# Kernel tuning notes

Measured on AMD Instinct MI355X. Metric: run time of the kernel, lower is better.

The kernel has to match this reference:

```python
import jax, jax.numpy as jnp
import numpy as np

D_MODEL = 1024
N_HEADS = 16
N_KV_HEADS = 4
HEAD_DIM = 64


def setup_inputs() -> dict:
    key = jax.random.key(0)
    ks = jax.random.split(key, 5)
    B, T, P = 2, 512, 8
    scale = 1.0 / np.sqrt(D_MODEL)
    return {
        "hidden_states": jax.random.normal(ks[0], (B, T, P, D_MODEL), dtype=jnp.float32),
        # weights stored [in, out] so y = x @ W (same math as nn.Linear with W^T)
        "Wq": jax.random.normal(ks[1], (D_MODEL, N_HEADS * HEAD_DIM), dtype=jnp.float32) * scale,
        "Wk": jax.random.normal(ks[2], (D_MODEL, N_KV_HEADS * HEAD_DIM), dtype=jnp.float32) * scale,
        "Wv": jax.random.normal(ks[3], (D_MODEL, N_KV_HEADS * HEAD_DIM), dtype=jnp.float32) * scale,
        "Wo": jax.random.normal(ks[4], (N_HEADS * HEAD_DIM, D_MODEL), dtype=jnp.float32) * scale,
    }


def _rope_tables(T, d):
    half = d // 2
    inv_freq = 1.0 / (10000.0 ** (jnp.arange(half, dtype=jnp.float32) / half))
    pos = jnp.arange(T, dtype=jnp.float32)
    angles = pos[:, None] * inv_freq[None, :]  # (T, half)
    return jnp.cos(angles), jnp.sin(angles)


def _apply_rope(x, cos, sin):
    # x: (B, P, T, H, d); cos/sin: (T, d/2)
    half = x.shape[-1] // 2
    x1, x2 = x[..., :half], x[..., half:]
    c = cos[None, None, :, None, :]
    s = sin[None, None, :, None, :]
    return jnp.concatenate([x1 * c - x2 * s, x1 * s + x2 * c], axis=-1)


def reference(hidden_states, Wq, Wk, Wv, Wo):
    B, T, P, _ = hidden_states.shape
    x = jnp.transpose(hidden_states, (0, 2, 1, 3))  # (B, P, T, C)
    q = (x @ Wq).reshape(B, P, T, N_HEADS, HEAD_DIM)
    k = (x @ Wk).reshape(B, P, T, N_KV_HEADS, HEAD_DIM)
    v = (x @ Wv).reshape(B, P, T, N_KV_HEADS, HEAD_DIM)

    rep = N_HEADS // N_KV_HEADS
    k = jnp.repeat(k, rep, axis=3)  # (B,P,T,H,d) interleaved like torch repeat/view
    v = jnp.repeat(v, rep, axis=3)

    cos, sin = _rope_tables(T, HEAD_DIM)
    q = _apply_rope(q, cos, sin)
    k = _apply_rope(k, cos, sin)

    # (B,P,H,T,d)
    q = jnp.transpose(q, (0, 1, 3, 2, 4))
    k = jnp.transpose(k, (0, 1, 3, 2, 4))
    v = jnp.transpose(v, (0, 1, 3, 2, 4))

    attn = jnp.einsum("bphqd,bphkd->bphqk", q, k) / jnp.sqrt(
        jnp.asarray(HEAD_DIM, q.dtype))
    attn = jax.nn.softmax(attn, axis=-1)
    out = jnp.einsum("bphqk,bphkd->bphqd", attn, v)
    out = jnp.transpose(out, (0, 1, 3, 2, 4)).reshape(B, P, T, N_HEADS * HEAD_DIM)
    out = jnp.transpose(out, (0, 2, 1, 3))  # (B, T, P, H*d)
    return out @ Wo
```

## Files before the change

kernel.cpp:

```cpp
#include <hip/hip_runtime.h>
#include <stdint.h>


typedef __attribute__((ext_vector_type(8))) short bf16x8;
typedef __attribute__((ext_vector_type(4))) float f32x4;
typedef __attribute__((ext_vector_type(16))) float f32x16;
typedef __attribute__((ext_vector_type(4))) unsigned short us4;
typedef __attribute__((ext_vector_type(8))) unsigned short us8;

static __device__ __forceinline__ unsigned short f2bf(float f) {
  unsigned u = __float_as_uint(f);
  u += 0x7fffu + ((u >> 16) & 1u);
  return (unsigned short)(u >> 16);
}

static __device__ __forceinline__ void ld_lds16(const void* g, void* l) {
  __builtin_amdgcn_global_load_lds(
      (const __attribute__((address_space(1))) void*)g,
      (__attribute__((address_space(3))) void*)l, 16, 0, 0);
}

static __device__ __forceinline__ f32x4 mfma16(bf16x8 a, bf16x8 b, f32x4 c) {
  return __builtin_amdgcn_mfma_f32_16x16x32_bf16(a, b, c, 0, 0, 0);
}
static __device__ __forceinline__ f32x16 mfma32(bf16x8 a, bf16x8 b, f32x16 c) {
  return __builtin_amdgcn_mfma_f32_32x32x16_bf16(a, b, c, 0, 0, 0);
}

__global__ __launch_bounds__(256) void conv_all(
    const float* __restrict__ hs, const float* __restrict__ Wq,
    const float* __restrict__ Wk, const float* __restrict__ Wv,
    const float* __restrict__ Wo, unsigned short* __restrict__ xb,
    unsigned short* __restrict__ wqkv, unsigned short* __restrict__ wot) {
  __shared__ float tile[64][65];
  int bid = blockIdx.x, tid = threadIdx.x;
  if (bid < 8192) {
    int gid = bid * 256 + tid;
    size_t e = (size_t)gid * 4;
    int r = (int)(e >> 10);
    int d = (int)(e & 1023);
    int b = r >> 12, p = (r >> 9) & 7, t = r & 511;
    const float4* src = (const float4*)(hs + ((((size_t)b * 512 + t) * 8 + p) << 10) + d);
    float4 v = *src;
    us4 o;
    o.x = f2bf(v.x); o.y = f2bf(v.y); o.z = f2bf(v.z); o.w = f2bf(v.w);
    *(us4*)(xb + e) = o;
    return;
  }
  int tb = bid - 8192;
  const float* W; unsigned short* Wt; int N, tc0, tn0;
  if (tb < 256)      { W = Wq; Wt = wqkv;                       N = 1024; tc0 = (tb >> 4) * 64;          tn0 = (tb & 15) * 64; }
  else if (tb < 320) { W = Wk; Wt = wqkv + (size_t)1024 * 1024; N = 256;  tc0 = ((tb - 256) >> 2) * 64;  tn0 = ((tb - 256) & 3) * 64; }
  else if (tb < 384) { W = Wv; Wt = wqkv + (size_t)1280 * 1024; N = 256;  tc0 = ((tb - 320) >> 2) * 64;  tn0 = ((tb - 320) & 3) * 64; }
  else               { W = Wo; Wt = wot;                        N = 1024; tc0 = ((tb - 384) >> 4) * 64;  tn0 = ((tb - 384) & 15) * 64; }
  int tr = tid >> 4, tc = tid & 15;
#pragma unroll
  for (int i = 0; i < 4; ++i) {
    int c = tr + i * 16;
    float4 v = *(const float4*)(W + (size_t)(tc0 + c) * N + tn0 + tc * 4);
    tile[c][tc * 4 + 0] = v.x; tile[c][tc * 4 + 1] = v.y;
    tile[c][tc * 4 + 2] = v.z; tile[c][tc * 4 + 3] = v.w;
  }
  __syncthreads();
#pragma unroll
  for (int i = 0; i < 4; ++i) {
    int n = tr + i * 16;
    us4 o;
    o.x = f2bf(tile[tc * 4 + 0][n]); o.y = f2bf(tile[tc * 4 + 1][n]);
    o.z = f2bf(tile[tc * 4 + 2][n]); o.w = f2bf(tile[tc * 4 + 3][n]);
    *(us4*)(Wt + (size_t)(tn0 + n) * 1024 + tc0 + tc * 4) = o;
  }
}

template <int NT, int MODE>
__global__ __launch_bounds__(512, 2) void gemm256(
    const unsigned short* __restrict__ A, const unsigned short* __restrict__ Bt,
    unsigned short* __restrict__ qb, unsigned short* __restrict__ kb,
    unsigned short* __restrict__ vtb, float* __restrict__ out) {
  constexpr int K = 1024;
  constexpr int KT = K / 64;
  __shared__ __align__(16) unsigned short Sm[2][2][256 * 64];
  unsigned short* Cs = &Sm[0][0][0];

  int tid = threadIdx.x;
  int lane = tid & 63, wid = tid >> 6;
  int quad = lane >> 4, lo = lane & 15;
  int tn = blockIdx.x % NT, tm = blockIdx.x / NT;
  int wr = wid >> 2, wc = wid & 3;
  int srow = lane >> 3, schunk = lane & 7;
  int cg = schunk ^ srow;

  const unsigned short* pa = A + ((size_t)(tm * 256) + wid * 8 + srow) * K + cg * 8;
  const unsigned short* pb = Bt + ((size_t)(tn * 256) + wid * 8 + srow) * K + cg * 8;

  f32x4 z = {0.f, 0.f, 0.f, 0.f};
  f32x4 acc[8][4];
#pragma unroll
  for (int i = 0; i < 8; ++i)
#pragma unroll
    for (int j = 0; j < 4; ++j) acc[i][j] = z;

  auto stage = [&](int t, int p) {
#pragma unroll
    for (int i = 0; i < 4; ++i) {
      ld_lds16(pa + (size_t)i * 64 * K + t * 64,
               (char*)&Sm[p][0][0] + (wid * 8 + i * 64) * 128);
      ld_lds16(pb + (size_t)i * 64 * K + t * 64,
               (char*)&Sm[p][1][0] + (wid * 8 + i * 64) * 128);
    }
  };

  stage(0, 0);
  stage(1, 1);
  asm volatile("s_waitcnt vmcnt(8)" ::: "memory");
  asm volatile("s_barrier" ::: "memory");

  bf16x8 af[4][2], bb0[2][2], bb1[2][2];

  for (int t = 0; t < KT; ++t) {
    int p = t & 1;
    const unsigned short* As = &Sm[p][0][0];
    const unsigned short* Bs = &Sm[p][1][0];

#pragma unroll
    for (int mi = 0; mi < 4; ++mi)
#pragma unroll
      for (int kx = 0; kx < 2; ++kx) {
        int row = wr * 128 + mi * 16 + lo;
        int cgx = (quad + kx * 4) ^ (row & 7);
        af[mi][kx] = *(const bf16x8*)(As + (size_t)row * 64 + cgx * 8);
      }
#pragma unroll
    for (int ni = 0; ni < 2; ++ni)
#pragma unroll
      for (int kx = 0; kx < 2; ++kx) {
        int row = wc * 64 + ni * 16 + lo;
        int cgx = (quad + kx * 4) ^ (row & 7);
        bb0[ni][kx] = *(const bf16x8*)(Bs + (size_t)row * 64 + cgx * 8);
      }
    asm volatile("s_barrier" ::: "memory");
    __builtin_amdgcn_s_setprio(1);
#pragma unroll
    for (int kx = 0; kx < 2; ++kx)
#pragma unroll
      for (int mi = 0; mi < 4; ++mi)
#pragma unroll
        for (int ni = 0; ni < 2; ++ni)
          acc[mi][ni] = mfma16(af[mi][kx], bb0[ni][kx], acc[mi][ni]);
    __builtin_amdgcn_s_setprio(0);
    asm volatile("s_barrier" ::: "memory");

#pragma unroll
    for (int ni = 0; ni < 2; ++ni)
#pragma unroll
      for (int kx = 0; kx < 2; ++kx) {
        int row = wc * 64 + (ni + 2) * 16 + lo;
        int cgx = (quad + kx * 4) ^ (row & 7);
        bb1[ni][kx] = *(const bf16x8*)(Bs + (size_t)row * 64 + cgx * 8);
      }
    asm volatile("s_barrier" ::: "memory");
    __builtin_amdgcn_s_setprio(1);
#pragma unroll
    for (int kx = 0; kx < 2; ++kx)
#pragma unroll
      for (int mi = 0; mi < 4; ++mi)
#pragma unroll
        for (int ni = 0; ni < 2; ++ni)
          acc[mi][ni + 2] = mfma16(af[mi][kx], bb1[ni][kx], acc[mi][ni + 2]);
    __builtin_amdgcn_s_setprio(0);
    asm volatile("s_barrier" ::: "memory");

#pragma unroll
    for (int mi = 0; mi < 4; ++mi)
#pragma unroll
      for (int kx = 0; kx < 2; ++kx) {
        int row = wr * 128 + 64 + mi * 16 + lo;
        int cgx = (quad + kx * 4) ^ (row & 7);
        af[mi][kx] = *(const bf16x8*)(As + (size_t)row * 64 + cgx * 8);
      }
    asm volatile("s_barrier" ::: "memory");
    __builtin_amdgcn_s_setprio(1);
#pragma unroll
    for (int kx = 0; kx < 2; ++kx)
#pragma unroll
      for (int mi = 0; mi < 4; ++mi)
#pragma unroll
        for (int ni = 0; ni < 2; ++ni)
          acc[mi + 4][ni + 2] = mfma16(af[mi][kx], bb1[ni][kx], acc[mi + 4][ni + 2]);
    __builtin_amdgcn_s_setprio(0);
    asm volatile("s_barrier" ::: "memory");

    bool pf = (t + 2 < KT);
    if (pf) stage(t + 2, p);
    __builtin_amdgcn_s_setprio(1);
#pragma unroll
    for (int kx = 0; kx < 2; ++kx)
#pragma unroll
      for (int mi = 0; mi < 4; ++mi)
#pragma unroll
        for (int ni = 0; ni < 2; ++ni)
          acc[mi + 4][ni] = mfma16(af[mi][kx], bb0[ni][kx], acc[mi + 4][ni]);
    __builtin_amdgcn_s_setprio(0);
    if (pf) asm volatile("s_waitcnt vmcnt(8)" ::: "memory");
    else    asm volatile("s_waitcnt vmcnt(0)" ::: "memory");
    asm volatile("s_barrier" ::: "memory");
  }

  if (MODE == 0 && tn < 5) {
    float qscale = (tn < 4) ? 0.125f : 1.0f;
#pragma unroll
    for (int mi = 0; mi < 8; ++mi)
#pragma unroll
      for (int r = 0; r < 4; ++r) {
        int row = wr * 128 + mi * 16 + quad * 4 + r;
        int tpos = (tm * 256 + row) & 511;
#pragma unroll
        for (int ni = 0; ni < 2; ++ni) {
          float invf = exp2f((float)(ni * 16 + lo) * -0.41524101186092029f);
          float ang = (float)tpos * invf;
          float s, c;
          __sincosf(ang, &s, &c);
          float x1 = acc[mi][ni][r], x2 = acc[mi][ni + 2][r];
          acc[mi][ni][r]     = (x1 * c - x2 * s) * qscale;
          acc[mi][ni + 2][r] = (x1 * s + x2 * c) * qscale;
        }
      }
#pragma unroll
    for (int mi = 0; mi < 8; ++mi)
#pragma unroll
      for (int ni = 0; ni < 4; ++ni)
#pragma unroll
        for (int r = 0; r < 4; ++r) {
          int row = wr * 128 + mi * 16 + quad * 4 + r;
          int col = wc * 64 + ni * 16 + lo;
          int cs = col ^ (((row >> 2) & 3) << 3);
          Cs[row * 256 + cs] = f2bf(acc[mi][ni][r]);
        }
    __syncthreads();
    int tc = tid & 31, ro = tid >> 5;
#pragma unroll
    for (int it = 0; it < 16; ++it) {
      int row = ro + 16 * it;
      int cs = (tc * 8) ^ (((row >> 2) & 3) << 3);
      us8 v = *(const us8*)(Cs + row * 256 + cs);
      size_t grow = (size_t)(tm * 256 + row);
      if (tn < 4) *(us8*)(qb + grow * 1024 + tn * 256 + tc * 8) = v;
      else        *(us8*)(kb + grow * 256 + tc * 8) = v;
    }
  } else if (MODE == 0) {
#pragma unroll
    for (int mi = 0; mi < 8; ++mi)
#pragma unroll
      for (int ni = 0; ni < 4; ++ni)
#pragma unroll
        for (int r = 0; r < 4; ++r) {
          int trow = wr * 128 + mi * 16 + quad * 4 + r;
          int col = wc * 64 + ni * 16 + lo;
          Cs[col * 256 + (trow ^ ((col & 7) << 3))] = f2bf(acc[mi][ni][r]);
        }
    __syncthreads();
    int t0 = (tid & 31) * 8, colIdx = tid >> 5;
    int bp = tm >> 1, tbase = (tm & 1) * 256;
#pragma unroll
    for (int it = 0; it < 16; ++it) {
      int col = colIdx + it * 16;
      us8 v = *(const us8*)(Cs + col * 256 + (t0 ^ ((col & 7) << 3)));
      int hh = col >> 6, dd = col & 63;
      *(us8*)(vtb + (((size_t)(bp * 4 + hh)) * 64 + dd) * 512 + tbase + t0) = v;
    }
  } else {
#pragma unroll
    for (int mi = 0; mi < 8; ++mi) {
      for (int ni = 0; ni < 4; ++ni) {
        int col = tn * 256 + wc * 64 + ni * 16 + lo;
        for (int r = 0; r < 4; ++r) {
          int grow = tm * 256 + wr * 128 + mi * 16 + quad * 4 + r;
          int bp = grow >> 9, tt = grow & 511;
          int b = bp >> 3, pp = bp & 7;
          out[((((size_t)b * 512 + tt) * 8 + pp) << 10) + col] = acc[mi][ni][r];
        }
      }
    }
  }
}

__global__ __launch_bounds__(256, 4) void attn(
    const unsigned short* __restrict__ qb, const unsigned short* __restrict__ kb,
    const unsigned short* __restrict__ vtb, unsigned short* __restrict__ ao) {
  __shared__ __align__(16) unsigned short Qs[128 * 64];
  __shared__ __align__(16) unsigned short Ks[64 * 64];
  __shared__ __align__(16) unsigned short Vs[64 * 64];

  int tid = threadIdx.x;
  int lane = tid & 63, wid = tid >> 6;
  int lo32 = lane & 31, hl = lane >> 5;
  int qt = blockIdx.x & 3, bph = blockIdx.x >> 2;
  int head = bph & 15, bp = bph >> 4;
  int kvh = head >> 2;
  int t0 = qt * 128;
  int srow = lane >> 3, schunk = lane & 7;

  const unsigned short* qg = qb + ((size_t)(bp * 512 + t0)) * 1024 + head * 64;
  const unsigned short* kg = kb + ((size_t)bp * 512) * 256 + kvh * 64;
  const unsigned short* vg = vtb + ((size_t)(bp * 4 + kvh)) * 64 * 512;

  for (int i = 0; i < 4; ++i) {
    int row = wid * 8 + i * 32 + srow;
    int cg = schunk ^ (row & 7);
    ld_lds16(qg + (size_t)row * 1024 + cg * 8, (char*)Qs + (wid * 8 + i * 32) * 128);
  }

  f32x16 z16 = {0.f};
  f32x16 o0 = z16, o1 = z16;
  float psum = 0.f;
  int qrow = wid * 32 + lo32;

  for (int kt = 0; kt < 512; kt += 64) {
    __syncthreads();
    for (int i = 0; i < 2; ++i) {
      int row = wid * 8 + i * 32 + srow;
      int cg = schunk ^ (row & 7);
      ld_lds16(kg + (size_t)(kt + row) * 256 + cg * 8, (char*)Ks + (wid * 8 + i * 32) * 128);
      ld_lds16(vg + (size_t)row * 512 + kt + cg * 8, (char*)Vs + (wid * 8 + i * 32) * 128);
    }
    __syncthreads();

    f32x16 st0 = z16, st1 = z16;
#pragma unroll
    for (int kkc = 0; kkc < 4; ++kkc) {
      int ch = 2 * kkc + hl;
      bf16x8 qf = *(const bf16x8*)(Qs + (size_t)qrow * 64 + ((ch ^ (qrow & 7)) * 8));
      bf16x8 kf0 = *(const bf16x8*)(Ks + (size_t)lo32 * 64 + ((ch ^ (lo32 & 7)) * 8));
      bf16x8 kf1 = *(const bf16x8*)(Ks + (size_t)(32 + lo32) * 64 + ((ch ^ (lo32 & 7)) * 8));
      st0 = mfma32(kf0, qf, st0);
      st1 = mfma32(kf1, qf, st1);
    }

#pragma unroll
    for (int t = 0; t < 2; ++t) {
      const f32x16& stv = t ? st1 : st0;
      unsigned pk[8], xpk[8];
#pragma unroll
      for (int p = 0; p < 8; ++p) {
        float e0 = __expf(stv[2 * p]);
        float e1 = __expf(stv[2 * p + 1]);
        psum += e0 + e1;
        pk[p] = ((__float_as_uint(e0) + 0x8000u) >> 16) |
                ((__float_as_uint(e1) + 0x8000u) & 0xffff0000u);
      }
#pragma unroll
      for (int p = 0; p < 8; ++p) xpk[p] = (unsigned)__shfl_xor((int)pk[p], 32);
#pragma unroll
      for (int cc = 0; cc < 2; ++cc) {
        int o = cc * 4;
        union { unsigned u[4]; bf16x8 v; } af;
        if (hl == 0) {
          af.u[0] = pk[o];      af.u[1] = pk[o + 1];
          af.u[2] = xpk[o];     af.u[3] = xpk[o + 1];
        } else {
          af.u[0] = xpk[o + 2]; af.u[1] = xpk[o + 3];
          af.u[2] = pk[o + 2];  af.u[3] = pk[o + 3];
        }
        int vch = 2 * (t * 2 + cc) + hl;
        bf16x8 v0 = *(const bf16x8*)(Vs + (size_t)lo32 * 64 + ((vch ^ (lo32 & 7)) * 8));
        bf16x8 v1 = *(const bf16x8*)(Vs + (size_t)(32 + lo32) * 64 + ((vch ^ (lo32 & 7)) * 8));
        o0 = mfma32(af.v, v0, o0);
        o1 = mfma32(af.v, v1, o1);
      }
    }
  }

  psum += __shfl_xor(psum, 32);
  float inv = 1.f / psum;
#pragma unroll
  for (int r = 0; r < 16; ++r) {
    int q_r = (r & 3) + 8 * (r >> 2) + 4 * hl;
    float sc = __shfl(inv, q_r);
    size_t grow = (size_t)(bp * 512 + t0 + wid * 32 + q_r);
    ao[grow * 1024 + head * 64 + lo32]      = f2bf(o0[r] * sc);
    ao[grow * 1024 + head * 64 + 32 + lo32] = f2bf(o1[r] * sc);
  }
}

extern "C" void kernel_launch(void* const* d_in, const int* in_sizes, int n_in,
                              void* d_out, int out_size, void* d_ws, size_t ws_size,
                              hipStream_t stream) {
  const float* hs = (const float*)d_in[0];
  const float* Wq = (const float*)d_in[1];
  const float* Wk = (const float*)d_in[2];
  const float* Wv = (const float*)d_in[3];
  const float* Wo = (const float*)d_in[4];
  float* out = (float*)d_out;

  unsigned short* xb   = (unsigned short*)d_ws;
  unsigned short* wqkv = xb + (size_t)8192 * 1024;
  unsigned short* wot  = wqkv + (size_t)1536 * 1024;
  unsigned short* qbuf = wot + (size_t)1024 * 1024;
  unsigned short* kbuf = qbuf + (size_t)8192 * 1024;
  unsigned short* vtb  = kbuf + (size_t)8192 * 256;
  unsigned short* ao   = xb;

  conv_all<<<8832, 256, 0, stream>>>(hs, Wq, Wk, Wv, Wo, xb, wqkv, wot);
  gemm256<6, 0><<<192, 512, 0, stream>>>(xb, wqkv, qbuf, kbuf, vtb, nullptr);
  attn<<<1024, 256, 0, stream>>>(qbuf, kbuf, vtb, ao);
  gemm256<4, 1><<<128, 512, 0, stream>>>(ao, wot, nullptr, nullptr, nullptr, out);
}
```

Before: 191.8 us.

## Split output GEMM into 128x256 tiles and remap block IDs across XCDs

After: 179.5 us. 6.4% less time.

```diff
diff --git a/kernel.cpp b/kernel.cpp
--- a/kernel.cpp
+++ b/kernel.cpp
@@ -72,11 +72,10 @@
   }
 }
 
-template <int NT, int MODE>
-__global__ __launch_bounds__(512, 2) void gemm256(
+__global__ __launch_bounds__(512, 2) void gemm_qkv(
     const unsigned short* __restrict__ A, const unsigned short* __restrict__ Bt,
     unsigned short* __restrict__ qb, unsigned short* __restrict__ kb,
-    unsigned short* __restrict__ vtb, float* __restrict__ out) {
+    unsigned short* __restrict__ vtb) {
   constexpr int K = 1024;
   constexpr int KT = K / 64;
   __shared__ __align__(16) unsigned short Sm[2][2][256 * 64];
@@ -85,7 +84,8 @@
   int tid = threadIdx.x;
   int lane = tid & 63, wid = tid >> 6;
   int quad = lane >> 4, lo = lane & 15;
-  int tn = blockIdx.x % NT, tm = blockIdx.x / NT;
+  int wg = (blockIdx.x & 7) * 24 + (blockIdx.x >> 3);
+  int tn = wg % 6, tm = wg / 6;
   int wr = wid >> 2, wc = wid & 3;
   int srow = lane >> 3, schunk = lane & 7;
   int cg = schunk ^ srow;
@@ -206,7 +206,7 @@
     asm volatile("s_barrier" ::: "memory");
   }
 
-  if (MODE == 0 && tn < 5) {
+  if (tn < 5) {
     float qscale = (tn < 4) ? 0.125f : 1.0f;
 #pragma unroll
     for (int mi = 0; mi < 8; ++mi)
@@ -247,7 +247,7 @@
       if (tn < 4) *(us8*)(qb + grow * 1024 + tn * 256 + tc * 8) = v;
       else        *(us8*)(kb + grow * 256 + tc * 8) = v;
     }
-  } else if (MODE == 0) {
+  } else {
 #pragma unroll
     for (int mi = 0; mi < 8; ++mi)
 #pragma unroll
@@ -268,17 +268,127 @@
       int hh = col >> 6, dd = col & 63;
       *(us8*)(vtb + (((size_t)(bp * 4 + hh)) * 64 + dd) * 512 + tbase + t0) = v;
     }
-  } else {
-#pragma unroll
-    for (int mi = 0; mi < 8; ++mi) {
-      for (int ni = 0; ni < 4; ++ni) {
-        int col = tn * 256 + wc * 64 + ni * 16 + lo;
-        for (int r = 0; r < 4; ++r) {
-          int grow = tm * 256 + wr * 128 + mi * 16 + quad * 4 + r;
-          int bp = grow >> 9, tt = grow & 511;
-          int b = bp >> 3, pp = bp & 7;
-          out[((((size_t)b * 512 + tt) * 8 + pp) << 10) + col] = acc[mi][ni][r];
-        }
+  }
+}
+
+__global__ __launch_bounds__(512, 2) void gemm_o(
+    const unsigned short* __restrict__ A, const unsigned short* __restrict__ Bt,
+    float* __restrict__ out) {
+  constexpr int K = 1024;
+  constexpr int KT = K / 64;
+  __shared__ __align__(16) unsigned short Sm[2][(128 + 256) * 64];
+
+  int tid = threadIdx.x;
+  int lane = tid & 63, wid = tid >> 6;
+  int quad = lane >> 4, lo = lane & 15;
+  int wg = (blockIdx.x & 7) * 32 + (blockIdx.x >> 3);
+  int tn = wg & 3, tm = wg >> 2;
+  int wr = wid >> 2, wc = wid & 3;
+  int srow = lane >> 3, schunk = lane & 7;
+  int cg = schunk ^ srow;
+
+  const unsigned short* pa = A + ((size_t)(tm * 128) + wid * 8 + srow) * K + cg * 8;
+  const unsigned short* pb = Bt + ((size_t)(tn * 256) + wid * 8 + srow) * K + cg * 8;
+
+  f32x4 z = {0.f, 0.f, 0.f, 0.f};
+  f32x4 acc[4][4];
+#pragma unroll
+  for (int i = 0; i < 4; ++i)
+#pragma unroll
+    for (int j = 0; j < 4; ++j) acc[i][j] = z;
+
+  auto stage = [&](int t, int p) {
+    unsigned short* As = &Sm[p][0];
+    unsigned short* Bs = &Sm[p][128 * 64];
+#pragma unroll
+    for (int i = 0; i < 2; ++i)
+      ld_lds16(pa + (size_t)i * 64 * K + t * 64,
+               (char*)As + (wid * 8 + i * 64) * 128);
+#pragma unroll
+    for (int i = 0; i < 4; ++i)
+      ld_lds16(pb + (size_t)i * 64 * K + t * 64,
+               (char*)Bs + (wid * 8 + i * 64) * 128);
+  };
+
+  stage(0, 0);
+  stage(1, 1);
+  asm volatile("s_waitcnt vmcnt(6)" ::: "memory");
+  asm volatile("s_barrier" ::: "memory");
+
+  bf16x8 af[4][2], bb0[2][2], bb1[2][2];
+
+  for (int t = 0; t < KT; ++t) {
+    int p = t & 1;
+    const unsigned short* As = &Sm[p][0];
+    const unsigned short* Bs = &Sm[p][128 * 64];
+
+#pragma unroll
+    for (int mi = 0; mi < 4; ++mi)
+#pragma unroll
+      for (int kx = 0; kx < 2; ++kx) {
+        int row = wr * 64 + mi * 16 + lo;
+        int cgx = (quad + kx * 4) ^ (row & 7);
+        af[mi][kx] = *(const bf16x8*)(As + (size_t)row * 64 + cgx * 8);
+      }
+#pragma unroll
+    for (int ni = 0; ni < 2; ++ni)
+#pragma unroll
+      for (int kx = 0; kx < 2; ++kx) {
+        int row = wc * 64 + ni * 16 + lo;
+        int cgx = (quad + kx * 4) ^ (row & 7);
+        bb0[ni][kx] = *(const bf16x8*)(Bs + (size_t)row * 64 + cgx * 8);
+      }
+    asm volatile("s_barrier" ::: "memory");
+    __builtin_amdgcn_s_setprio(1);
+#pragma unroll
+    for (int kx = 0; kx < 2; ++kx)
+#pragma unroll
+      for (int mi = 0; mi < 4; ++mi)
+#pragma unroll
+        for (int ni = 0; ni < 2; ++ni)
+          acc[mi][ni] = mfma16(af[mi][kx], bb0[ni][kx], acc[mi][ni]);
+    __builtin_amdgcn_s_setprio(0);
+    asm volatile("s_barrier" ::: "memory");
+
+#pragma unroll
+    for (int ni = 0; ni < 2; ++ni)
+#pragma unroll
+      for (int kx = 0; kx < 2; ++kx) {
+        int row = wc * 64 + (ni + 2) * 16 + lo;
+        int cgx = (quad + kx * 4) ^ (row & 7);
+        bb1[ni][kx] = *(const bf16x8*)(Bs + (size_t)row * 64 + cgx * 8);
+      }
+    asm volatile("s_barrier" ::: "memory");
+    __builtin_amdgcn_s_setprio(1);
+#pragma unroll
+    for (int kx = 0; kx < 2; ++kx)
+#pragma unroll
+      for (int mi = 0; mi < 4; ++mi)
+#pragma unroll
+        for (int ni = 0; ni < 2; ++ni)
+          acc[mi][ni + 2] = mfma16(af[mi][kx], bb1[ni][kx], acc[mi][ni + 2]);
+    __builtin_amdgcn_s_setprio(0);
+    asm volatile("s_barrier" ::: "memory");
+
+    bool pf = (t + 2 < KT);
+    if (pf) {
+      stage(t + 2, p);
+      asm volatile("s_waitcnt vmcnt(6)" ::: "memory");
+    } else {
+      asm volatile("s_waitcnt vmcnt(0)" ::: "memory");
+    }
+    asm volatile("s_barrier" ::: "memory");
+  }
+
+#pragma unroll
+  for (int mi = 0; mi < 4; ++mi) {
+    for (int ni = 0; ni < 4; ++ni) {
+      int col = tn * 256 + wc * 64 + ni * 16 + lo;
+      for (int r = 0; r < 4; ++r) {
+        int grow = tm * 128 + wr * 64 + mi * 16 + quad * 4 + r;
+        int bp = grow >> 9, tt = grow & 511;
+        int b = bp >> 3, pp = bp & 7;
+        out[((((size_t)b * 512 + tt) * 8 + pp) << 10) + col] = acc[mi][ni][r];
       }
     }
   }
@@ -294,7 +404,8 @@
   int tid = threadIdx.x;
   int lane = tid & 63, wid = tid >> 6;
   int lo32 = lane & 31, hl = lane >> 5;
-  int qt = blockIdx.x & 3, bph = blockIdx.x >> 2;
+  int wg = (blockIdx.x & 7) * 128 + (blockIdx.x >> 3);
+  int qt = wg & 3, bph = wg >> 2;
   int head = bph & 15, bp = bph >> 4;
   int kvh = head >> 2;
   int t0 = qt * 128;
@@ -401,7 +512,7 @@
   unsigned short* ao   = xb;
 
   conv_all<<<8832, 256, 0, stream>>>(hs, Wq, Wk, Wv, Wo, xb, wqkv, wot);
-  gemm256<6, 0><<<192, 512, 0, stream>>>(xb, wqkv, qbuf, kbuf, vtb, nullptr);
+  gemm_qkv<<<192, 512, 0, stream>>>(xb, wqkv, qbuf, kbuf, vtb);
   attn<<<1024, 256, 0, stream>>>(qbuf, kbuf, vtb, ao);
-  gemm256<4, 1><<<128, 512, 0, stream>>>(ao, wot, nullptr, nullptr, nullptr, out);
-}
+  gemm_o<<<256, 512, 0, stream>>>(ao, wot, out);
+}
```
